# Kernel optimization log

Hardware: AMD Instinct MI355X
Metric: run time of the kernel (lower is better)

The kernel has to match this reference:

```python
import jax, jax.numpy as jnp
import numpy as np

# Per-channel class frequencies from the original module (23 AU channels)
_W = np.array([0.0012597430655963838, 0.0004919313290455535, 0.0021106513104319356,
               0.0007678117365508301, 0.004719881670572202, 0.000372272357115554,
               0.029090425620315438, 0.010056339432617042, 0.0034817436971298467,
               0.0003057951504877765, 0.003995280118329428, 8.808229878180519e-05,
               0.012070598793438699, 0.016788818533845208, 0.0017832510677901316,
               0.0008758371973209686, 0.0005933090691529143, 0.0031992155689617922,
               0.003212511010287348, 0.0016685778863572154, 0.0009356666832859684,
               0.0010985358395240233, 0.00103372056306194], dtype=np.float32)
_WEIGHT_0 = 1.0 / (_W + 1.0)        # used when target == 0
_WEIGHT_1 = 1.0 - _WEIGHT_0          # used when target == 1

B, C = 1000000, 23

def setup_inputs() -> dict:
    key = jax.random.key(0)
    k1, k2 = jax.random.split(key)
    # probabilities strictly inside (0,1) so log terms stay finite
    x = jax.random.uniform(k1, (B, C), dtype=jnp.float32) * 0.98 + 0.01
    labels = jax.random.randint(k2, (B, C), 0, 2, dtype=jnp.int32)
    return {"x": x, "labels": labels}

def reference(x, labels):
    # target = (labels > 0).float(); the eq(999) mask in the original is computed but unused
    target = (labels > 0).astype(x.dtype)
    w0 = jnp.asarray(_WEIGHT_0, dtype=x.dtype)  # [C]
    w1 = jnp.asarray(_WEIGHT_1, dtype=x.dtype)  # [C]
    # per-element weight: 1/weight_0[ch] if target==0 else 1/weight_1[ch]
    w = jnp.where(target == 0, 1.0 / w0, 1.0 / w1)  # [B, C] via broadcast
    bce = -(target * jnp.log(x) + (1.0 - target) * jnp.log(1.0 - x))
    loss = jnp.sum(w * bce)
    n, c = x.shape
    return loss / (n * c)
```

## Files before the change

kernel.cpp:

```cpp
#include <hip/hip_runtime.h>
#include <utility>

#define NCH 23
#define CHUNK_V4 23
#define CHUNK_ELEMS 92

constexpr float c_W[NCH] = {
    0.0012597430655963838f, 0.0004919313290455535f, 0.0021106513104319356f,
    0.0007678117365508301f, 0.004719881670572202f,  0.000372272357115554f,
    0.029090425620315438f,  0.010056339432617042f,  0.0034817436971298467f,
    0.0003057951504877765f, 0.003995280118329428f,  8.808229878180519e-05f,
    0.012070598793438699f,  0.016788818533845208f,  0.0017832510677901316f,
    0.0008758371973209686f, 0.0005933090691529143f, 0.0031992155689617922f,
    0.003212511010287348f,  0.0016685778863572154f, 0.0009356666832859684f,
    0.0010985358395240233f, 0.00103372056306194f
};
constexpr float NEG_LN2 = -0.69314718055994530942f;

struct Tabs { float w0n[NCH]; float w1n[NCH]; };

constexpr Tabs make_tabs() {
    Tabs t{};
    for (int c = 0; c < NCH; ++c) {
        float w0 = 1.0f / (c_W[c] + 1.0f);
        float w1 = 1.0f - w0;
        t.w0n[c] = (1.0f / w0) * NEG_LN2;
        t.w1n[c] = (1.0f / w1) * NEG_LN2;
    }
    return t;
}

constexpr Tabs c_tabs = make_tabs();
__constant__ Tabs d_tabs = make_tabs();

__device__ __forceinline__ void elem(float xx, int lab, float w0n, float w1n,
                                     float& acc) {
    bool t  = lab > 0;
    float v = t ? xx : 1.0f - xx;
    float w = t ? w1n : w0n;
    acc = __builtin_fmaf(w, __log2f(v), acc);
}

template <int J>
__device__ __forceinline__ void do_vec4(const float4& xv, const int4& lv, float& acc) {
    elem(xv.x, lv.x, c_tabs.w0n[(4 * J + 0) % NCH], c_tabs.w1n[(4 * J + 0) % NCH], acc);
    elem(xv.y, lv.y, c_tabs.w0n[(4 * J + 1) % NCH], c_tabs.w1n[(4 * J + 1) % NCH], acc);
    elem(xv.z, lv.z, c_tabs.w0n[(4 * J + 2) % NCH], c_tabs.w1n[(4 * J + 2) % NCH], acc);
    elem(xv.w, lv.w, c_tabs.w0n[(4 * J + 3) % NCH], c_tabs.w1n[(4 * J + 3) % NCH], acc);
}

template <int... J>
__device__ __forceinline__ void do_chunk(const float4* __restrict__ xp,
                                         const int4* __restrict__ lp, float& acc,
                                         std::integer_sequence<int, J...>) {
    float4 xv[CHUNK_V4];
    int4   lv[CHUNK_V4];
    ((xv[J] = xp[J]), ...);
    ((lv[J] = lp[J]), ...);
    (do_vec4<J>(xv[J], lv[J], acc), ...);
}

__global__ __launch_bounds__(256) void bce_reduce_kernel(
        const float* __restrict__ x, const int* __restrict__ labels,
        double* __restrict__ partial, unsigned n) {
    const unsigned nchunks = n / CHUNK_ELEMS;
    const unsigned t = blockIdx.x * blockDim.x + threadIdx.x;
    float acc = 0.0f;

    if (t < nchunks) {
        const float4* xp = (const float4*)x + (size_t)t * CHUNK_V4;
        const int4*   lp = (const int4*)labels + (size_t)t * CHUNK_V4;
        do_chunk(xp, lp, acc, std::make_integer_sequence<int, CHUNK_V4>{});
    }

    const unsigned tail = nchunks * CHUNK_ELEMS;
    const unsigned nthreads = gridDim.x * blockDim.x;
    for (unsigned i = tail + t; i < n; i += nthreads) {
        unsigned c = i % NCH;
        elem(x[i], labels[i], d_tabs.w0n[c], d_tabs.w1n[c], acc);
    }

    #pragma unroll
    for (int off = 32; off > 0; off >>= 1) acc += __shfl_down(acc, off, 64);
    __shared__ float s_part[4];
    const int wave = threadIdx.x >> 6;
    const int lane = threadIdx.x & 63;
    if (lane == 0) s_part[wave] = acc;
    __syncthreads();
    if (threadIdx.x == 0) {
        float s = s_part[0] + s_part[1] + s_part[2] + s_part[3];
        atomicAdd(partial, (double)s);
    }
}

__global__ void bce_finalize_kernel(const double* __restrict__ partial,
                                    float* __restrict__ out, unsigned n) {
    out[0] = (float)(partial[0] / (double)n);
}

extern "C" void kernel_launch(void* const* d_in, const int* in_sizes, int n_in,
                              void* d_out, int out_size, void* d_ws, size_t ws_size,
                              hipStream_t stream) {
    const float* x      = (const float*)d_in[0];
    const int*   labels = (const int*)d_in[1];
    float*       out    = (float*)d_out;
    double*      acc    = (double*)d_ws;
    unsigned n = (unsigned)in_sizes[0];

    hipMemsetAsync(acc, 0, sizeof(double), stream);

    const unsigned nchunks = n / CHUNK_ELEMS;
    const int block = 256;
    const int grid  = (int)((nchunks + block - 1) / block);
    bce_reduce_kernel<<<grid, block, 0, stream>>>(x, labels, acc, n);
    bce_finalize_kernel<<<1, 1, 0, stream>>>(acc, out, n);
}
```

Measured before the change: 230.6 us.

## Use coalesced wave-strided float4 tiles with grid-stride loop and LDS weight table

Replaces the per-thread contiguous 92-element chunk, where each lane reads its own 368-byte span and accesses are strided across lanes, with wave-level tiles in which consecutive lanes read consecutive float4s. This gives coalesced global loads. A fixed grid of 1024 blocks walks the tiles in a grid-stride loop. Channel indices are computed at runtime with modular arithmetic, and the weights are read from a shared-memory table rather than compile-time constants. This adds LDS lookups and index arithmetic per element, and the tail loop assumes n is divisible by 4.

```diff
diff --git a/kernel.cpp b/kernel.cpp
--- a/kernel.cpp
+++ b/kernel.cpp
@@ -1,9 +1,8 @@
 #include <hip/hip_runtime.h>
-#include <utility>
 
 #define NCH 23
-#define CHUNK_V4 23
-#define CHUNK_ELEMS 92
+#define U 4
+#define TILE_V4 (64 * U)
 
 constexpr float c_W[NCH] = {
     0.0012597430655963838f, 0.0004919313290455535f, 0.0021106513104319356f,
@@ -17,75 +16,82 @@
 };
 constexpr float NEG_LN2 = -0.69314718055994530942f;
 
-struct Tabs { float w0n[NCH]; float w1n[NCH]; };
-
+struct Tabs { float w[2 * NCH]; };
 constexpr Tabs make_tabs() {
     Tabs t{};
     for (int c = 0; c < NCH; ++c) {
         float w0 = 1.0f / (c_W[c] + 1.0f);
         float w1 = 1.0f - w0;
-        t.w0n[c] = (1.0f / w0) * NEG_LN2;
-        t.w1n[c] = (1.0f / w1) * NEG_LN2;
+        t.w[c]       = (1.0f / w0) * NEG_LN2;
+        t.w[NCH + c] = (1.0f / w1) * NEG_LN2;
     }
     return t;
 }
-
-constexpr Tabs c_tabs = make_tabs();
 __constant__ Tabs d_tabs = make_tabs();
 
-__device__ __forceinline__ void elem(float xx, int lab, float w0n, float w1n,
-                                     float& acc) {
+__device__ __forceinline__ unsigned wrap23(unsigned c) {
+    return c >= NCH ? c - NCH : c;
+}
+
+__device__ __forceinline__ void elem(float xx, int lab, unsigned c,
+                                     const float* s_wt, float& acc) {
     bool t  = lab > 0;
     float v = t ? xx : 1.0f - xx;
-    float w = t ? w1n : w0n;
+    float w = s_wt[c + (t ? NCH : 0u)];
     acc = __builtin_fmaf(w, __log2f(v), acc);
 }
 
-template <int J>
-__device__ __forceinline__ void do_vec4(const float4& xv, const int4& lv, float& acc) {
-    elem(xv.x, lv.x, c_tabs.w0n[(4 * J + 0) % NCH], c_tabs.w1n[(4 * J + 0) % NCH], acc);
-    elem(xv.y, lv.y, c_tabs.w0n[(4 * J + 1) % NCH], c_tabs.w1n[(4 * J + 1) % NCH], acc);
-    elem(xv.z, lv.z, c_tabs.w0n[(4 * J + 2) % NCH], c_tabs.w1n[(4 * J + 2) % NCH], acc);
-    elem(xv.w, lv.w, c_tabs.w0n[(4 * J + 3) % NCH], c_tabs.w1n[(4 * J + 3) % NCH], acc);
-}
+__global__ __launch_bounds__(256) void bce_reduce_kernel(
+        const float4* __restrict__ x4, const int4* __restrict__ l4,
+        double* __restrict__ partial, unsigned n4 ) {
+    __shared__ float s_wt[2 * NCH];
+    if (threadIdx.x < 2 * NCH) s_wt[threadIdx.x] = d_tabs.w[threadIdx.x];
+    __syncthreads();
 
-template <int... J>
-__device__ __forceinline__ void do_chunk(const float4* __restrict__ xp,
-                                         const int4* __restrict__ lp, float& acc,
-                                         std::integer_sequence<int, J...>) {
-    float4 xv[CHUNK_V4];
-    int4   lv[CHUNK_V4];
-    ((xv[J] = xp[J]), ...);
-    ((lv[J] = lp[J]), ...);
-    (do_vec4<J>(xv[J], lv[J], acc), ...);
-}
+    const unsigned gtid     = blockIdx.x * blockDim.x + threadIdx.x;
+    const unsigned nthreads = gridDim.x * blockDim.x;
+    const unsigned lane     = threadIdx.x & 63u;
+    const unsigned wid      = gtid >> 6;
+    const unsigned nwaves   = nthreads >> 6;
+    const unsigned ntiles   = n4 / TILE_V4;
 
-__global__ __launch_bounds__(256) void bce_reduce_kernel(
-        const float* __restrict__ x, const int* __restrict__ labels,
-        double* __restrict__ partial, unsigned n) {
-    const unsigned nchunks = n / CHUNK_ELEMS;
-    const unsigned t = blockIdx.x * blockDim.x + threadIdx.x;
     float acc = 0.0f;
 
-    if (t < nchunks) {
-        const float4* xp = (const float4*)x + (size_t)t * CHUNK_V4;
-        const int4*   lp = (const int4*)labels + (size_t)t * CHUNK_V4;
-        do_chunk(xp, lp, acc, std::make_integer_sequence<int, CHUNK_V4>{});
+    for (unsigned T = wid; T < ntiles; T += nwaves) {
+        const unsigned base = T * TILE_V4;
+        float4 xv[U];
+        int4   lv[U];
+        #pragma unroll
+        for (int j = 0; j < U; ++j) xv[j] = x4[base + 64u * j + lane];
+        #pragma unroll
+        for (int j = 0; j < U; ++j) lv[j] = l4[base + 64u * j + lane];
+
+        const unsigned cb = (12u * T + 4u * lane) % NCH;
+        #pragma unroll
+        for (int j = 0; j < U; ++j) {
+            unsigned c = wrap23(cb + (3u * j) % NCH);
+            elem(xv[j].x, lv[j].x, c, s_wt, acc); c = wrap23(c + 1);
+            elem(xv[j].y, lv[j].y, c, s_wt, acc); c = wrap23(c + 1);
+            elem(xv[j].z, lv[j].z, c, s_wt, acc); c = wrap23(c + 1);
+            elem(xv[j].w, lv[j].w, c, s_wt, acc);
+        }
     }
 
-    const unsigned tail = nchunks * CHUNK_ELEMS;
-    const unsigned nthreads = gridDim.x * blockDim.x;
-    for (unsigned i = tail + t; i < n; i += nthreads) {
-        unsigned c = i % NCH;
-        elem(x[i], labels[i], d_tabs.w0n[c], d_tabs.w1n[c], acc);
+    for (unsigned v = ntiles * TILE_V4 + gtid; v < n4; v += nthreads) {
+        float4 xv = x4[v];
+        int4   lv = l4[v];
+        unsigned c = (4u * v) % NCH;
+        elem(xv.x, lv.x, c, s_wt, acc); c = wrap23(c + 1);
+        elem(xv.y, lv.y, c, s_wt, acc); c = wrap23(c + 1);
+        elem(xv.z, lv.z, c, s_wt, acc); c = wrap23(c + 1);
+        elem(xv.w, lv.w, c, s_wt, acc);
     }
 
     #pragma unroll
     for (int off = 32; off > 0; off >>= 1) acc += __shfl_down(acc, off, 64);
     __shared__ float s_part[4];
     const int wave = threadIdx.x >> 6;
-    const int lane = threadIdx.x & 63;
-    if (lane == 0) s_part[wave] = acc;
+    if ((threadIdx.x & 63) == 0) s_part[wave] = acc;
     __syncthreads();
     if (threadIdx.x == 0) {
         float s = s_part[0] + s_part[1] + s_part[2] + s_part[3];
@@ -105,13 +111,14 @@
     const int*   labels = (const int*)d_in[1];
     float*       out    = (float*)d_out;
     double*      acc    = (double*)d_ws;
-    unsigned n = (unsigned)in_sizes[0];
+    unsigned n  = (unsigned)in_sizes[0];
+    unsigned n4 = n >> 2;
 
     hipMemsetAsync(acc, 0, sizeof(double), stream);
 
-    const unsigned nchunks = n / CHUNK_ELEMS;
     const int block = 256;
-    const int grid  = (int)((nchunks + block - 1) / block);
-    bce_reduce_kernel<<<grid, block, 0, stream>>>(x, labels, acc, n);
+    const int grid  = 1024;
+    bce_reduce_kernel<<<grid, block, 0, stream>>>(
+        (const float4*)x, (const int4*)labels, acc, n4);
     bce_finalize_kernel<<<1, 1, 0, stream>>>(acc, out, n);
 }
```

New measurement: 197.9 us. 1.17x faster.
